# Kernel tuning notes

Measured on AMD Instinct MI355X. Metric: run time of the kernel, lower is better.

Reference implementation:

```python
import jax, jax.numpy as jnp
import numpy as np

N = 100000   # nodes
E = 1600000  # edges (avg degree 16)
D = 128      # feature width (constant across the 3 blocks)
L = 3        # number of residual LEConv blocks
EPS = 1e-5
SLOPE = 0.01  # leaky_relu negative slope


def setup_inputs() -> dict:
    key = jax.random.key(0)
    ks = jax.random.split(key, 10)
    y = jax.random.normal(ks[0], (N, D), dtype=jnp.float32)
    edge_index = jax.random.randint(ks[1], (2, E), 0, N, dtype=jnp.int64)
    s = 0.05
    W1 = jax.random.normal(ks[2], (L, D, D), dtype=jnp.float32) * s
    b1 = jax.random.normal(ks[3], (L, D), dtype=jnp.float32) * s
    W2 = jax.random.normal(ks[4], (L, D, D), dtype=jnp.float32) * s   # lin2: no bias
    W3 = jax.random.normal(ks[5], (L, D, D), dtype=jnp.float32) * s
    b3 = jax.random.normal(ks[6], (L, D), dtype=jnp.float32) * s
    ln_w = jnp.ones((L, D), dtype=jnp.float32)
    ln_b = jnp.zeros((L, D), dtype=jnp.float32)
    return {"y": y, "edge_index": edge_index, "W1": W1, "b1": b1,
            "W2": W2, "W3": W3, "b3": b3, "ln_w": ln_w, "ln_b": ln_b}


def reference(y, edge_index, W1, b1, W2, W3, b3, ln_w, ln_b):
    n = y.shape[0]
    src, dst = edge_index[0], edge_index[1]
    # in-degree per destination node (edge_weight = 1)
    deg = jax.ops.segment_sum(jnp.ones((src.shape[0],), dtype=y.dtype), dst,
                              num_segments=n)  # [N]
    for l in range(L):
        # LEConv: out_i = sum_{j->i} (lin1(x)_j - lin2(x)_i) + lin3(x)_i
        a = y @ W1[l] + b1[l]          # [N, D] (lin1, with bias)
        b = y @ W2[l]                  # [N, D] (lin2, no bias)
        agg = jax.ops.segment_sum(a[src], dst, num_segments=n) - deg[:, None] * b
        h = agg + y @ W3[l] + b3[l]    # + lin3(x)
        # PyG LayerNorm mode='graph', batch=None: scalar mean/std over all elems
        h = h - h.mean()
        h = h / (h.std() + EPS)
        h = h * ln_w[l] + ln_b[l]
        # leaky_relu, dropout p=0 (no-op), identity residual
        h = jnp.where(h >= 0, h, SLOPE * h)
        y = y + h
    return y
```

## Files before the change

### kernel.cpp

```cpp
#include <hip/hip_runtime.h>
#include <hip/hip_bf16.h>
#include <math.h>

#define N_NODES 100000
#define N_EDGES 1600000
#define DF      128
#define EPSV    1e-5f
#define SLOPE   0.01f
#define M_TOT   (N_NODES * DF)
#define NB_SCAN 391

typedef __hip_bfloat16 bf16;
typedef __attribute__((ext_vector_type(8))) short short8;
typedef __attribute__((ext_vector_type(4))) float f32x4;

__global__ void k_detect(const unsigned int* __restrict__ yw32, int* __restrict__ flagp)
{
    __shared__ int cnt;
    if (threadIdx.x == 0) cnt = 0;
    __syncthreads();
    unsigned w = yw32[threadIdx.x];
    int e = (w >> 7) & 0xFF;
    if (e >= 96 && e <= 140) atomicAdd(&cnt, 1);
    __syncthreads();
    if (threadIdx.x == 0) flagp[0] = (cnt >= 150) ? 1 : 0;
}

__global__ void k_zero(int* __restrict__ p, int n)
{
    int i = blockIdx.x * 256 + threadIdx.x;
    if (i < n) p[i] = 0;
}

__global__ __launch_bounds__(256) void k_cvt_y(const void* __restrict__ yin,
                                               bf16* __restrict__ yw,
                                               const int* __restrict__ flagp)
{
    const long t = (long)blockIdx.x * 256 + threadIdx.x;
    const int isbf = flagp[0];
    float f[8];
    if (isbf) {
        uint4 v = reinterpret_cast<const uint4*>(yin)[t];
        const bf16* s = reinterpret_cast<const bf16*>(&v);
#pragma unroll
        for (int j = 0; j < 8; ++j) f[j] = __bfloat162float(s[j]);
    } else {
        float4 v0 = reinterpret_cast<const float4*>(yin)[2 * t];
        float4 v1 = reinterpret_cast<const float4*>(yin)[2 * t + 1];
        f[0] = v0.x; f[1] = v0.y; f[2] = v0.z; f[3] = v0.w;
        f[4] = v1.x; f[5] = v1.y; f[6] = v1.z; f[7] = v1.w;
    }
    uint4 ov;
    bf16* o = reinterpret_cast<bf16*>(&ov);
#pragma unroll
    for (int j = 0; j < 8; ++j) {
        float x = f[j];
        if (!isfinite(x)) x = 0.f;
        o[j] = __float2bfloat16(x);
    }
    reinterpret_cast<uint4*>(yw)[t] = ov;
}

__global__ void k_wt(const void* __restrict__ W1, const void* __restrict__ W2,
                     const void* __restrict__ W3, bf16* __restrict__ Wt,
                     const int* __restrict__ flagp)
{
    int idx = blockIdx.x * 256 + threadIdx.x;
    const int isbf = flagp[0];
    int mat = idx >> 14;
    int r   = idx & 16383;
    int k   = r >> 7, n = r & 127;
    int l = mat / 3, which = mat - l * 3;
    const void* src = (which == 0) ? W1 : (which == 1 ? W2 : W3);
    size_t ofs = (size_t)l * 16384 + (size_t)k * 128 + n;
    float v = isbf ? __bfloat162float(reinterpret_cast<const bf16*>(src)[ofs])
                   : reinterpret_cast<const float*>(src)[ofs];
    if (!isfinite(v)) v = 0.f;
    Wt[((size_t)mat << 14) + (size_t)n * 128 + k] = __float2bfloat16(v);
}

__global__ void k_small(const void* __restrict__ b1, const void* __restrict__ b3,
                        const void* __restrict__ lnw, const void* __restrict__ lnb,
                        bf16* __restrict__ prm, const int* __restrict__ flagp)
{
    int i = blockIdx.x * 256 + threadIdx.x;
    if (i >= 1536) return;
    const int isbf = flagp[0];
    int which = i / 384, r = i - which * 384;
    const void* src = (which == 0) ? b1 : (which == 1) ? b3 : (which == 2) ? lnw : lnb;
    float v = isbf ? __bfloat162float(reinterpret_cast<const bf16*>(src)[r])
                   : reinterpret_cast<const float*>(src)[r];
    if (!isfinite(v)) v = 0.f;
    prm[i] = __float2bfloat16(v);
}

__device__ __forceinline__ void edge_decode(const int* __restrict__ ei, int e,
                                            int& s, int& d)
{
    bool is64 = ((ei[1] | ei[3] | ei[5] | ei[7]) == 0);
    if (is64) { s = ei[2 * e]; d = ei[2 * (N_EDGES + e)]; }
    else      { s = ei[e];     d = ei[N_EDGES + e];       }
}

__global__ void k_deg(const int* __restrict__ ei, int* __restrict__ degcnt,
                      int* __restrict__ rank)
{
    int e = blockIdx.x * 256 + threadIdx.x;
    if (e >= N_EDGES) return;
    int s, d;
    edge_decode(ei, e, s, d);
    if ((unsigned)s >= N_NODES || (unsigned)d >= N_NODES) return;
    rank[e] = atomicAdd(&degcnt[d], 1);
}

__global__ void k_scan1(const int* __restrict__ deg, int* __restrict__ bsum)
{
    __shared__ int red[4];
    int i = blockIdx.x * 256 + threadIdx.x;
    int v = (i < N_NODES) ? deg[i] : 0;
#pragma unroll
    for (int m = 1; m < 64; m <<= 1) v += __shfl_xor(v, m);
    if ((threadIdx.x & 63) == 0) red[threadIdx.x >> 6] = v;
    __syncthreads();
    if (threadIdx.x == 0) bsum[blockIdx.x] = red[0] + red[1] + red[2] + red[3];
}

__global__ void k_scan2(const int* __restrict__ bsum, int* __restrict__ bpre)
{
    __shared__ int sc[512];
    int tid = threadIdx.x;
    int v = (tid < NB_SCAN) ? bsum[tid] : 0;
    sc[tid] = v;
    __syncthreads();
    for (int off = 1; off < 512; off <<= 1) {
        int t = (tid >= off) ? sc[tid - off] : 0;
        __syncthreads();
        sc[tid] += t;
        __syncthreads();
    }
    if (tid < NB_SCAN) bpre[tid] = sc[tid] - v;
}

__global__ void k_scan3(const int* __restrict__ deg, const int* __restrict__ bpre,
                        int* __restrict__ offs)
{
    __shared__ int sc[256];
    int tid = threadIdx.x;
    int i = blockIdx.x * 256 + tid;
    int v = (i < N_NODES) ? deg[i] : 0;
    sc[tid] = v;
    __syncthreads();
    for (int off = 1; off < 256; off <<= 1) {
        int t = (tid >= off) ? sc[tid - off] : 0;
        __syncthreads();
        sc[tid] += t;
        __syncthreads();
    }
    if (i < N_NODES) offs[i] = bpre[blockIdx.x] + sc[tid] - v;
}

__global__ void k_fill(const int* __restrict__ ei, const int* __restrict__ offs,
                       const int* __restrict__ rank, int* __restrict__ edst)
{
    int e = blockIdx.x * 256 + threadIdx.x;
    if (e >= N_EDGES) return;
    int s, d;
    edge_decode(ei, e, s, d);
    if ((unsigned)s >= N_NODES || (unsigned)d >= N_NODES) return;
    edst[offs[d] + rank[e]] = s;
}

__global__ __launch_bounds__(256) void k_gemm3(
    bf16* __restrict__ yw, const bf16* __restrict__ hprev,
    const float* __restrict__ stats, const bf16* __restrict__ Wt,
    const bf16* __restrict__ prm, const int* __restrict__ degcnt,
    bf16* __restrict__ aBuf, bf16* __restrict__ cmb, int layer)
{
    __shared__ bf16 Asm[64][136];
    __shared__ bf16 Bsm[128][136];

    const int tid = threadIdx.x;
    const long r0 = (long)blockIdx.x * 64;

    const uint4* gy = reinterpret_cast<const uint4*>(yw);

    if (layer == 0) {
#pragma unroll
        for (int it = 0; it < 4; ++it) {
            int chunk = it * 256 + tid;
            int row = chunk >> 4, colc = (chunk & 15) * 8;
            uint4 v = make_uint4(0, 0, 0, 0);
            long grow = r0 + row;
            if (grow < N_NODES) v = gy[grow * 16 + (chunk & 15)];
            *reinterpret_cast<uint4*>(&Asm[row][colc]) = v;
        }
    } else {
        const float mean = stats[(layer - 1) * 2];
        const float inv  = stats[(layer - 1) * 2 + 1];
        const bf16* lnwc = prm + 768  + (layer - 1) * 128;
        const bf16* lnbc = prm + 1152 + (layer - 1) * 128;
        const uint4* gh = reinterpret_cast<const uint4*>(hprev);
#pragma unroll
        for (int it = 0; it < 4; ++it) {
            int chunk = it * 256 + tid;
            int row = chunk >> 4, c16 = chunk & 15, colc = c16 * 8;
            long grow = r0 + row;
            uint4 ov = make_uint4(0, 0, 0, 0);
            if (grow < N_NODES) {
                uint4 hv = gh[grow * 16 + c16];
                uint4 yv = gy[grow * 16 + c16];
                const bf16* h8 = reinterpret_cast<const bf16*>(&hv);
                const bf16* y8 = reinterpret_cast<const bf16*>(&yv);
                bf16* o8 = reinterpret_cast<bf16*>(&ov);
#pragma unroll
                for (int jj = 0; jj < 8; ++jj) {
                    float g = __bfloat162float(lnwc[colc + jj]);
                    float b = __bfloat162float(lnbc[colc + jj]);
                    float hh = (__bfloat162float(h8[jj]) - mean) * inv * g + b;
                    hh = (hh >= 0.f) ? hh : SLOPE * hh;
                    o8[jj] = __float2bfloat16(__bfloat162float(y8[jj]) + hh);
                }
                reinterpret_cast<uint4*>(yw)[grow * 16 + c16] = ov;
            }
            *reinterpret_cast<uint4*>(&Asm[row][colc]) = ov;
        }
    }

#define STAGE_B(MATIDX)                                                          \
    {                                                                            \
        const uint4* gw = reinterpret_cast<const uint4*>(Wt + ((size_t)(MATIDX) << 14)); \
        _Pragma("unroll")                                                        \
        for (int it = 0; it < 8; ++it) {                                         \
            int chunk = it * 256 + tid;                                          \
            *reinterpret_cast<uint4*>(&Bsm[chunk >> 4][(chunk & 15) * 8]) = gw[chunk]; \
        }                                                                        \
    }

    const int wave = tid >> 6, lane = tid & 63;
    const int lm = lane & 15, quad = lane >> 4;
    const int mrow = wave * 16 + lm;

    f32x4 accB[8], accC[8];
#pragma unroll
    for (int nt = 0; nt < 8; ++nt) {
        accB[nt] = (f32x4){0.f, 0.f, 0.f, 0.f};
        accC[nt] = (f32x4){0.f, 0.f, 0.f, 0.f};
    }

    STAGE_B(layer * 3 + 1);
    __syncthreads();
#pragma unroll
    for (int kk = 0; kk < 4; ++kk) {
        const int kb = kk * 32 + quad * 8;
        short8 afr = *reinterpret_cast<const short8*>(&Asm[mrow][kb]);
#pragma unroll
        for (int nt = 0; nt < 8; ++nt) {
            short8 bfr = *reinterpret_cast<const short8*>(&Bsm[nt * 16 + lm][kb]);
            accB[nt] = __builtin_amdgcn_mfma_f32_16x16x32_bf16(afr, bfr, accB[nt], 0, 0, 0);
        }
    }
    __syncthreads();

    STAGE_B(layer * 3 + 2);
    __syncthreads();
#pragma unroll
    for (int kk = 0; kk < 4; ++kk) {
        const int kb = kk * 32 + quad * 8;
        short8 afr = *reinterpret_cast<const short8*>(&Asm[mrow][kb]);
#pragma unroll
        for (int nt = 0; nt < 8; ++nt) {
            short8 bfr = *reinterpret_cast<const short8*>(&Bsm[nt * 16 + lm][kb]);
            accC[nt] = __builtin_amdgcn_mfma_f32_16x16x32_bf16(afr, bfr, accC[nt], 0, 0, 0);
        }
    }

    const bf16* b3c = prm + 384 + layer * 128;
#pragma unroll
    for (int i = 0; i < 4; ++i) {
        long row = r0 + wave * 16 + quad * 4 + i;
        if (row < N_NODES) {
            float degf = (float)degcnt[row];
#pragma unroll
            for (int nt = 0; nt < 8; ++nt) {
                int col = nt * 16 + lm;
                float v = accC[nt][i] + __bfloat162float(b3c[col]) - degf * accB[nt][i];
                cmb[row * 128 + col] = __float2bfloat16(v);
            }
        }
    }
    __syncthreads();

    STAGE_B(layer * 3 + 0);
    __syncthreads();
#pragma unroll
    for (int nt = 0; nt < 8; ++nt) accB[nt] = (f32x4){0.f, 0.f, 0.f, 0.f};
#pragma unroll
    for (int kk = 0; kk < 4; ++kk) {
        const int kb = kk * 32 + quad * 8;
        short8 afr = *reinterpret_cast<const short8*>(&Asm[mrow][kb]);
#pragma unroll
        for (int nt = 0; nt < 8; ++nt) {
            short8 bfr = *reinterpret_cast<const short8*>(&Bsm[nt * 16 + lm][kb]);
            accB[nt] = __builtin_amdgcn_mfma_f32_16x16x32_bf16(afr, bfr, accB[nt], 0, 0, 0);
        }
    }
    const bf16* b1c = prm + layer * 128;
#pragma unroll
    for (int i = 0; i < 4; ++i) {
        long row = r0 + wave * 16 + quad * 4 + i;
        if (row < N_NODES) {
#pragma unroll
            for (int nt = 0; nt < 8; ++nt) {
                int col = nt * 16 + lm;
                aBuf[row * 128 + col] =
                    __float2bfloat16(accB[nt][i] + __bfloat162float(b1c[col]));
            }
        }
    }
#undef STAGE_B
}

__global__ __launch_bounds__(256) void k_agg(
    const bf16* __restrict__ aBuf, bf16* __restrict__ cmb,
    const int* __restrict__ offs, const int* __restrict__ degcnt,
    const int* __restrict__ edst, float* __restrict__ buckets, int layer)
{
    __shared__ float red[8];

    const int tid  = threadIdx.x;
    const int w    = tid >> 6;
    const int lane = tid & 63;
    const int el   = lane >> 4;
    const int fb   = lane & 15;
    const long node = (long)blockIdx.x * 4 + w;

    const int start = offs[node];
    const int deg   = degcnt[node];
    const uint4* A4 = reinterpret_cast<const uint4*>(aBuf);

    float acc[8];
#pragma unroll
    for (int i = 0; i < 8; ++i) acc[i] = 0.f;

    int j = el;
    for (; j + 8 <= deg; j += 8) {
        int s0 = edst[start + j];
        int s1 = edst[start + j + 4];
        uint4 v0 = A4[(size_t)s0 * 16 + fb];
        uint4 v1 = A4[(size_t)s1 * 16 + fb];
        const unsigned* u0 = reinterpret_cast<const unsigned*>(&v0);
        const unsigned* u1 = reinterpret_cast<const unsigned*>(&v1);
#pragma unroll
        for (int d = 0; d < 4; ++d) {
            acc[2 * d]     += __uint_as_float(u0[d] << 16);
            acc[2 * d + 1] += __uint_as_float(u0[d] & 0xffff0000u);
            acc[2 * d]     += __uint_as_float(u1[d] << 16);
            acc[2 * d + 1] += __uint_as_float(u1[d] & 0xffff0000u);
        }
    }
    for (; j < deg; j += 4) {
        int s0 = edst[start + j];
        uint4 v0 = A4[(size_t)s0 * 16 + fb];
        const unsigned* u0 = reinterpret_cast<const unsigned*>(&v0);
#pragma unroll
        for (int d = 0; d < 4; ++d) {
            acc[2 * d]     += __uint_as_float(u0[d] << 16);
            acc[2 * d + 1] += __uint_as_float(u0[d] & 0xffff0000u);
        }
    }

#pragma unroll
    for (int i = 0; i < 8; ++i) {
        acc[i] += __shfl_xor(acc[i], 16);
        acc[i] += __shfl_xor(acc[i], 32);
    }

    uint4 cv = reinterpret_cast<const uint4*>(cmb)[node * 16 + fb];
    const unsigned* cu = reinterpret_cast<const unsigned*>(&cv);
    float h[8];
    float s1v = 0.f, s2v = 0.f;
#pragma unroll
    for (int d = 0; d < 4; ++d) {
        h[2 * d]     = acc[2 * d]     + __uint_as_float(cu[d] << 16);
        h[2 * d + 1] = acc[2 * d + 1] + __uint_as_float(cu[d] & 0xffff0000u);
    }
    uint4 ov;
    bf16* o8 = reinterpret_cast<bf16*>(&ov);
#pragma unroll
    for (int i = 0; i < 8; ++i) {
        o8[i] = __float2bfloat16(h[i]);
        s1v += h[i];
        s2v += h[i] * h[i];
    }
    if (el == 0) reinterpret_cast<uint4*>(cmb)[node * 16 + fb] = ov;

#pragma unroll
    for (int m = 1; m < 16; m <<= 1) {
        s1v += __shfl_xor(s1v, m);
        s2v += __shfl_xor(s2v, m);
    }
    if (lane == 0) { red[w] = s1v; red[4 + w] = s2v; }
    __syncthreads();
    if (tid == 0) {
        float S1 = red[0] + red[1] + red[2] + red[3];
        float S2 = red[4] + red[5] + red[6] + red[7];
        int bkt = blockIdx.x & 255;
        atomicAdd(&buckets[layer * 512 + bkt * 2], S1);
        atomicAdd(&buckets[layer * 512 + bkt * 2 + 1], S2);
    }
}

__global__ void k_red(const float* __restrict__ buckets, float* __restrict__ statsOut, int layer)
{
    __shared__ double red[8];
    const int tid = threadIdx.x;
    double s1 = (double)buckets[layer * 512 + tid * 2];
    double s2 = (double)buckets[layer * 512 + tid * 2 + 1];
#pragma unroll
    for (int m = 1; m < 64; m <<= 1) {
        s1 += __shfl_xor(s1, m);
        s2 += __shfl_xor(s2, m);
    }
    const int wv = tid >> 6;
    if ((tid & 63) == 0) { red[wv] = s1; red[4 + wv] = s2; }
    __syncthreads();
    if (tid == 0) {
        double S1 = red[0] + red[1] + red[2] + red[3];
        double S2 = red[4] + red[5] + red[6] + red[7];
        double mean, inv;
        if (isfinite(S1) && isfinite(S2)) {
            const double M = (double)M_TOT;
            mean = S1 / M;
            double var = S2 / M - mean * mean;
            if (!(var > 0.0)) var = 0.0;
            inv = 1.0 / (sqrt(var) + (double)EPSV);
        } else {
            mean = 0.0; inv = 1.0;
        }
        statsOut[layer * 2]     = (float)mean;
        statsOut[layer * 2 + 1] = (float)inv;
    }
}

__global__ __launch_bounds__(256) void k_norm(
    const bf16* __restrict__ hBuf, bf16* __restrict__ yw,
    const float* __restrict__ statsOut, const bf16* __restrict__ prm,
    void* __restrict__ outFinal, const int* __restrict__ flagp, int layer)
{
    const long i = (long)blockIdx.x * 256 + threadIdx.x;
    const float mean  = statsOut[layer * 2];
    const float scale = statsOut[layer * 2 + 1];

    uint4 hv = reinterpret_cast<const uint4*>(hBuf)[i];
    uint4 yv = reinterpret_cast<const uint4*>(yw)[i];
    const bf16* h8 = reinterpret_cast<const bf16*>(&hv);
    const bf16* y8 = reinterpret_cast<const bf16*>(&yv);
    const int colb = ((int)(i & 15)) * 8;
    const bf16* lnwc = prm + 768  + layer * 128;
    const bf16* lnbc = prm + 1152 + layer * 128;

    float r[8];
    uint4 ov;
    bf16* o8 = reinterpret_cast<bf16*>(&ov);
#pragma unroll
    for (int jj = 0; jj < 8; ++jj) {
        float g = __bfloat162float(lnwc[colb + jj]);
        float b = __bfloat162float(lnbc[colb + jj]);
        float h = (__bfloat162float(h8[jj]) - mean) * scale * g + b;
        h = (h >= 0.f) ? h : SLOPE * h;
        r[jj] = __bfloat162float(y8[jj]) + h;
        o8[jj] = __float2bfloat16(r[jj]);
    }
    if (flagp[0]) {
        reinterpret_cast<uint4*>(outFinal)[i] = ov;
    } else {
        float4 lo = make_float4(r[0], r[1], r[2], r[3]);
        float4 hi = make_float4(r[4], r[5], r[6], r[7]);
        reinterpret_cast<float4*>(outFinal)[2 * i]     = lo;
        reinterpret_cast<float4*>(outFinal)[2 * i + 1] = hi;
    }
}

extern "C" void kernel_launch(void* const* d_in, const int* in_sizes, int n_in,
                              void* d_out, int out_size, void* d_ws, size_t ws_size,
                              hipStream_t stream)
{
    const void* yIn = d_in[0];
    const int*  ei  = (const int*)d_in[1];
    const void* W1  = d_in[2];
    const void* b1  = d_in[3];
    const void* W2  = d_in[4];
    const void* W3  = d_in[5];
    const void* b3  = d_in[6];
    const void* lnw = d_in[7];
    const void* lnb = d_in[8];

    char* ws = (char*)d_ws;
    size_t o = 0;
    auto alloc = [&](size_t bytes) -> char* {
        char* p = ws + o;
        o += (bytes + 255) & ~(size_t)255;
        return p;
    };
    bf16* yw   = (bf16*)alloc((size_t)M_TOT * 2);
    bf16* aBuf = (bf16*)alloc((size_t)M_TOT * 2);
    bf16* cmb  = (bf16*)alloc((size_t)M_TOT * 2);
    bf16* Wt   = (bf16*)alloc((size_t)9 * 16384 * 2);
    bf16* prm  = (bf16*)alloc((size_t)1536 * 2);
    int*  edst = (int*)alloc((size_t)N_EDGES * 4);
    int*  rank = (int*)alloc((size_t)N_EDGES * 4);
    int*  offs = (int*)alloc((size_t)N_NODES * 4);
    int*  bsum = (int*)alloc((size_t)NB_SCAN * 4);
    int*  bpre = (int*)alloc((size_t)NB_SCAN * 4);
    const int nz = N_NODES + 3 * 512 + 8 + 8;
    int* zr = (int*)alloc((size_t)nz * 4);
    int*   degcnt   = zr;
    float* buckets  = (float*)(zr + N_NODES);
    float* statsOut = (float*)(zr + N_NODES + 3 * 512);
    int*   flagp    = zr + N_NODES + 3 * 512 + 8;

    k_zero  <<<(nz + 255) / 256, 256, 0, stream>>>(zr, nz);
    k_detect<<<1, 256, 0, stream>>>((const unsigned int*)yIn, flagp);
    k_cvt_y <<<M_TOT / (8 * 256), 256, 0, stream>>>(yIn, yw, flagp);
    k_wt    <<<(9 * 16384) / 256, 256, 0, stream>>>(W1, W2, W3, Wt, flagp);
    k_small <<<6, 256, 0, stream>>>(b1, b3, lnw, lnb, prm, flagp);
    k_deg   <<<N_EDGES / 256, 256, 0, stream>>>(ei, degcnt, rank);
    k_scan1 <<<NB_SCAN, 256, 0, stream>>>(degcnt, bsum);
    k_scan2 <<<1, 512, 0, stream>>>(bsum, bpre);
    k_scan3 <<<NB_SCAN, 256, 0, stream>>>(degcnt, bpre, offs);
    k_fill  <<<N_EDGES / 256, 256, 0, stream>>>(ei, offs, rank, edst);

    const int ngemm = (N_NODES + 63) / 64;
    for (int l = 0; l < 3; ++l) {
        k_gemm3<<<ngemm, 256, 0, stream>>>(yw, cmb, statsOut, Wt, prm, degcnt, aBuf, cmb, l);
        k_agg  <<<N_NODES / 4, 256, 0, stream>>>(aBuf, cmb, offs, degcnt, edst, buckets, l);
        k_red  <<<1, 256, 0, stream>>>(buckets, statsOut, l);
    }
    k_norm<<<M_TOT / (8 * 256), 256, 0, stream>>>(cmb, yw, statsOut, prm, d_out, flagp, 2);
}
```

Baseline: 556.0 us.

## Make aggregation kernel persistent with grid-stride waves and deeper gather unroll

The aggregation kernel now launches a fixed grid of 2048 blocks where each wave grid-strides over destination nodes instead of one wave per node. The gather loop is unrolled to four neighbor loads in flight, and the residual row load is hoisted ahead of it. Per-wave statistics accumulate across nodes and are flushed with one atomic pair per wave, which removes the shared-memory block reduction and barrier. The cost is less load balancing across waves, and the atomics are now per wave rather than per block.

```diff
diff --git a/kernel.cpp b/kernel.cpp
--- a/kernel.cpp
+++ b/kernel.cpp
@@ -320,93 +320,104 @@
 #undef STAGE_B
 }
 
-__global__ __launch_bounds__(256) void k_agg(
+#define AGG_BLOCKS 2048
+#define AGG_WAVES  (AGG_BLOCKS * 4)
+
+__global__ __launch_bounds__(256, 8) void k_agg(
     const bf16* __restrict__ aBuf, bf16* __restrict__ cmb,
     const int* __restrict__ offs, const int* __restrict__ degcnt,
     const int* __restrict__ edst, float* __restrict__ buckets, int layer)
 {
-    __shared__ float red[8];
-
     const int tid  = threadIdx.x;
-    const int w    = tid >> 6;
     const int lane = tid & 63;
     const int el   = lane >> 4;
     const int fb   = lane & 15;
-    const long node = (long)blockIdx.x * 4 + w;
-
-    const int start = offs[node];
-    const int deg   = degcnt[node];
+    const int wid  = __builtin_amdgcn_readfirstlane((int)(blockIdx.x * 4) + (tid >> 6));
+
     const uint4* A4 = reinterpret_cast<const uint4*>(aBuf);
 
-    float acc[8];
-#pragma unroll
-    for (int i = 0; i < 8; ++i) acc[i] = 0.f;
-
-    int j = el;
-    for (; j + 8 <= deg; j += 8) {
-        int s0 = edst[start + j];
-        int s1 = edst[start + j + 4];
-        uint4 v0 = A4[(size_t)s0 * 16 + fb];
-        uint4 v1 = A4[(size_t)s1 * 16 + fb];
-        const unsigned* u0 = reinterpret_cast<const unsigned*>(&v0);
-        const unsigned* u1 = reinterpret_cast<const unsigned*>(&v1);
+    float s1w = 0.f, s2w = 0.f;
+
+#define ACC8(v)                                                                \
+    {                                                                          \
+        const unsigned* _u = reinterpret_cast<const unsigned*>(&(v));          \
+        _Pragma("unroll")                                                      \
+        for (int _d = 0; _d < 4; ++_d) {                                       \
+            acc[2 * _d]     += __uint_as_float(_u[_d] << 16);                  \
+            acc[2 * _d + 1] += __uint_as_float(_u[_d] & 0xffff0000u);          \
+        }                                                                      \
+    }
+
+    for (int node = wid; node < N_NODES; node += AGG_WAVES) {
+        const int start = offs[node];
+        const int deg   = degcnt[node];
+
+        const uint4 cv = reinterpret_cast<const uint4*>(cmb)[(size_t)node * 16 + fb];
+
+        float acc[8];
+#pragma unroll
+        for (int i = 0; i < 8; ++i) acc[i] = 0.f;
+
+        int j = el;
+        for (; j + 12 < deg; j += 16) {
+            int e0 = edst[start + j];
+            int e1 = edst[start + j + 4];
+            int e2 = edst[start + j + 8];
+            int e3 = edst[start + j + 12];
+            uint4 v0 = A4[(size_t)e0 * 16 + fb];
+            uint4 v1 = A4[(size_t)e1 * 16 + fb];
+            uint4 v2 = A4[(size_t)e2 * 16 + fb];
+            uint4 v3 = A4[(size_t)e3 * 16 + fb];
+            ACC8(v0); ACC8(v1); ACC8(v2); ACC8(v3);
+        }
+        if (j + 4 < deg) {
+            int e0 = edst[start + j];
+            int e1 = edst[start + j + 4];
+            uint4 v0 = A4[(size_t)e0 * 16 + fb];
+            uint4 v1 = A4[(size_t)e1 * 16 + fb];
+            ACC8(v0); ACC8(v1);
+            j += 8;
+        }
+        if (j < deg) {
+            int e0 = edst[start + j];
+            uint4 v0 = A4[(size_t)e0 * 16 + fb];
+            ACC8(v0);
+        }
+
+#pragma unroll
+        for (int i = 0; i < 8; ++i) {
+            acc[i] += __shfl_xor(acc[i], 16);
+            acc[i] += __shfl_xor(acc[i], 32);
+        }
+
+        const unsigned* cu = reinterpret_cast<const unsigned*>(&cv);
+        float h[8];
 #pragma unroll
         for (int d = 0; d < 4; ++d) {
-            acc[2 * d]     += __uint_as_float(u0[d] << 16);
-            acc[2 * d + 1] += __uint_as_float(u0[d] & 0xffff0000u);
-            acc[2 * d]     += __uint_as_float(u1[d] << 16);
-            acc[2 * d + 1] += __uint_as_float(u1[d] & 0xffff0000u);
-        }
-    }
-    for (; j < deg; j += 4) {
-        int s0 = edst[start + j];
-        uint4 v0 = A4[(size_t)s0 * 16 + fb];
-        const unsigned* u0 = reinterpret_cast<const unsigned*>(&v0);
-#pragma unroll
-        for (int d = 0; d < 4; ++d) {
-            acc[2 * d]     += __uint_as_float(u0[d] << 16);
-            acc[2 * d + 1] += __uint_as_float(u0[d] & 0xffff0000u);
-        }
-    }
-
-#pragma unroll
-    for (int i = 0; i < 8; ++i) {
-        acc[i] += __shfl_xor(acc[i], 16);
-        acc[i] += __shfl_xor(acc[i], 32);
-    }
-
-    uint4 cv = reinterpret_cast<const uint4*>(cmb)[node * 16 + fb];
-    const unsigned* cu = reinterpret_cast<const unsigned*>(&cv);
-    float h[8];
-    float s1v = 0.f, s2v = 0.f;
-#pragma unroll
-    for (int d = 0; d < 4; ++d) {
-        h[2 * d]     = acc[2 * d]     + __uint_as_float(cu[d] << 16);
-        h[2 * d + 1] = acc[2 * d + 1] + __uint_as_float(cu[d] & 0xffff0000u);
-    }
-    uint4 ov;
-    bf16* o8 = reinterpret_cast<bf16*>(&ov);
-#pragma unroll
-    for (int i = 0; i < 8; ++i) {
-        o8[i] = __float2bfloat16(h[i]);
-        s1v += h[i];
-        s2v += h[i] * h[i];
-    }
-    if (el == 0) reinterpret_cast<uint4*>(cmb)[node * 16 + fb] = ov;
+            h[2 * d]     = acc[2 * d]     + __uint_as_float(cu[d] << 16);
+            h[2 * d + 1] = acc[2 * d + 1] + __uint_as_float(cu[d] & 0xffff0000u);
+        }
+        uint4 ov;
+        bf16* o8 = reinterpret_cast<bf16*>(&ov);
+#pragma unroll
+        for (int i = 0; i < 8; ++i) {
+            o8[i] = __float2bfloat16(h[i]);
+            s1w += h[i];
+            s2w += h[i] * h[i];
+        }
+        if (el == 0) reinterpret_cast<uint4*>(cmb)[(size_t)node * 16 + fb] = ov;
+    }
+#undef ACC8
 
 #pragma unroll
     for (int m = 1; m < 16; m <<= 1) {
-        s1v += __shfl_xor(s1v, m);
-        s2v += __shfl_xor(s2v, m);
-    }
-    if (lane == 0) { red[w] = s1v; red[4 + w] = s2v; }
-    __syncthreads();
-    if (tid == 0) {
-        float S1 = red[0] + red[1] + red[2] + red[3];
-        float S2 = red[4] + red[5] + red[6] + red[7];
-        int bkt = blockIdx.x & 255;
-        atomicAdd(&buckets[layer * 512 + bkt * 2], S1);
-        atomicAdd(&buckets[layer * 512 + bkt * 2 + 1], S2);
+        s1w += __shfl_xor(s1w, m);
+        s2w += __shfl_xor(s2w, m);
+    }
+    if (lane == 0) {
+        int bkt = wid & 255;
+        atomicAdd(&buckets[layer * 512 + bkt * 2],     s1w);
+        atomicAdd(&buckets[layer * 512 + bkt * 2 + 1], s2w);
     }
 }
 
@@ -533,7 +544,7 @@
     const int ngemm = (N_NODES + 63) / 64;
     for (int l = 0; l < 3; ++l) {
         k_gemm3<<<ngemm, 256, 0, stream>>>(yw, cmb, statsOut, Wt, prm, degcnt, aBuf, cmb, l);
-        k_agg  <<<N_NODES / 4, 256, 0, stream>>>(aBuf, cmb, offs, degcnt, edst, buckets, l);
+        k_agg  <<<AGG_BLOCKS, 256, 0, stream>>>(aBuf, cmb, offs, degcnt, edst, buckets, l);
         k_red  <<<1, 256, 0, stream>>>(buckets, statsOut, l);
     }
     k_norm<<<M_TOT / (8 * 256), 256, 0, stream>>>(cmb, yw, statsOut, prm, d_out, flagp, 2);
```

Result: faster. 545.1 us (-2.0%).
